# Kernel optimization log

Measured on AMD Instinct MI355X. Metric: run time of the kernel, lower is better.

The kernel has to match this reference:

```python
import jax, jax.numpy as jnp
import numpy as np

UNITS = 256


def setup_inputs() -> dict:
    key = jax.random.key(0)
    ks = jax.random.split(key, 9)
    B, H, W, C = 8, 64, 64, UNITS
    x = jax.random.normal(ks[0], (B, H, W, C), dtype=jnp.float32)
    # 1x1 Conv2D == per-pixel linear: weight [C_in, C_out], bias [C_out]
    def lin(k):
        return jax.random.normal(k, (C, UNITS), dtype=jnp.float32) * (2.0 / C) ** 0.5
    return {
        "x": x,
        "wq": lin(ks[1]), "bq": jnp.zeros((UNITS,), jnp.float32),
        "wk": lin(ks[2]), "bk": jnp.zeros((UNITS,), jnp.float32),
        "wv": lin(ks[3]), "bv": jnp.zeros((UNITS,), jnp.float32),
        "wp": lin(ks[4]), "bp": jnp.zeros((UNITS,), jnp.float32),
    }


def reference(x, wq, bq, wk, bk, wv, bv, wp, bp):
    B, H, W, C = x.shape
    N = H * W
    scale = jnp.asarray(UNITS, jnp.float32) ** -0.5
    xf = x.reshape(B, N, C)  # 1x1 conv == matmul over channels
    q = xf @ wq + bq
    k = xf @ wk + bk
    v = xf @ wv + bv
    # (b,h,w,c)x(b,H,W,c)->(b,h,w,H,W) flattened to (b,N,N)
    scores = jnp.einsum('bnc,bmc->bnm', q, k) * scale
    attn = jax.nn.softmax(scores, axis=-1)
    out = jnp.einsum('bnm,bmc->bnc', attn, v)
    proj = out @ wp + bp
    return x + proj.reshape(B, H, W, UNITS)
```

## Files before the change

kernel.cpp:

```cpp
#include <hip/hip_runtime.h>


typedef _Float16 half8 __attribute__((ext_vector_type(8)));
typedef _Float16 half4 __attribute__((ext_vector_type(4)));
typedef float f32x4 __attribute__((ext_vector_type(4)));
typedef float f32x16 __attribute__((ext_vector_type(16)));
typedef unsigned int u32x4 __attribute__((ext_vector_type(4)));
typedef unsigned int u32x2 __attribute__((ext_vector_type(2)));

#define MFMA16(a, b, c) __builtin_amdgcn_mfma_f32_16x16x32_f16((a), (b), (c), 0, 0, 0)
#define MFMA32(a, b, c) __builtin_amdgcn_mfma_f32_32x32x16_f16((a), (b), (c), 0, 0, 0)

#if __has_builtin(__builtin_amdgcn_exp2f)
#define EXP2(x) __builtin_amdgcn_exp2f(x)
#else
#define EXP2(x) exp2f(x)
#endif

#define QSCALE 0.09016843898f
#define ESHIFT 11.5415603f

__device__ __forceinline__ void lds_load16(const void* g, void* l) {
    __builtin_amdgcn_global_load_lds(
        (const __attribute__((address_space(1))) unsigned int*)g,
        (__attribute__((address_space(3))) unsigned int*)l, 16, 0, 0);
}

__global__ __launch_bounds__(256)
void wt_prep(const float* __restrict__ w0, const float* __restrict__ w1,
             const float* __restrict__ w2, const float* __restrict__ w3,
             _Float16* __restrict__ outw)
{
    __shared__ _Float16 sT[64 * 72];
    const int z = blockIdx.z;
    const float* W = (z == 0) ? w0 : (z == 1) ? w1 : (z == 2) ? w2 : w3;
    _Float16* O = outw + z * 65536;
    const int kb = blockIdx.x * 64, nb = blockIdx.y * 64;
    const int t = threadIdx.x;
    const int r = t >> 4, c4 = (t & 15) * 4;
#pragma unroll
    for (int i = 0; i < 4; ++i) {
        f32x4 ld = *(const f32x4*)(W + (size_t)(kb + r + i * 16) * 256 + nb + c4);
#pragma unroll
        for (int j = 0; j < 4; ++j) sT[(c4 + j) * 72 + r + i * 16] = (_Float16)ld[j];
    }
    __syncthreads();
#pragma unroll
    for (int i = 0; i < 4; ++i) {
        int n = r + i * 16;
        *(u32x2*)&O[(size_t)(nb + n) * 256 + kb + c4] = *(const u32x2*)&sT[n * 72 + c4];
    }
}

__global__ __launch_bounds__(256)
void qkv_gemm(const float* __restrict__ x, const _Float16* __restrict__ wt,
              const float* __restrict__ bq, const float* __restrict__ bk,
              const float* __restrict__ bv,
              _Float16* __restrict__ qo, _Float16* __restrict__ ko,
              _Float16* __restrict__ vo)
{
    __shared__ _Float16 smem[12800];

    const int tid  = threadIdx.x;
    const int w    = tid >> 6;
    const int lane = tid & 63;
    const int quad = lane >> 4;
    const int l16  = lane & 15;
    const int m0   = blockIdx.x * 128;
    const int n0   = blockIdx.y * 64;
    const int rA = tid >> 1, cA = (tid & 1) << 4;
    const int rB = tid >> 2, cB = (tid & 3) << 3;

    const float* ap = x + (size_t)(m0 + rA) * 256 + cA;
    f32x4 a0 = *(const f32x4*)ap,       a1 = *(const f32x4*)(ap + 4);
    f32x4 a2 = *(const f32x4*)(ap + 8), a3 = *(const f32x4*)(ap + 12);
    u32x4 bst[3];
#pragma unroll
    for (int o = 0; o < 3; ++o)
        bst[o] = *(const u32x4*)(wt + o * 65536 + (size_t)(n0 + rB) * 256 + cB);

    f32x4 zero4 = {0.f, 0.f, 0.f, 0.f};
    f32x4 acc[3][8];
#pragma unroll
    for (int o = 0; o < 3; ++o)
#pragma unroll
        for (int mt = 0; mt < 8; ++mt) acc[o][mt] = zero4;

    for (int it = 0; it < 8; ++it) {
        __syncthreads();
        half8 t0, t1;
#pragma unroll
        for (int j = 0; j < 4; ++j) {
            t0[j] = (_Float16)a0[j]; t0[j + 4] = (_Float16)a1[j];
            t1[j] = (_Float16)a2[j]; t1[j + 4] = (_Float16)a3[j];
        }
        *(half8*)&smem[rA * 40 + cA]     = t0;
        *(half8*)&smem[rA * 40 + cA + 8] = t1;
#pragma unroll
        for (int o = 0; o < 3; ++o)
            *(u32x4*)&smem[5120 + o * 2560 + rB * 40 + cB] = bst[o];
        __syncthreads();
        if (it < 7) {
            int k0 = (it + 1) * 32;
            const float* ap2 = x + (size_t)(m0 + rA) * 256 + k0 + cA;
            a0 = *(const f32x4*)ap2;       a1 = *(const f32x4*)(ap2 + 4);
            a2 = *(const f32x4*)(ap2 + 8); a3 = *(const f32x4*)(ap2 + 12);
#pragma unroll
            for (int o = 0; o < 3; ++o)
                bst[o] = *(const u32x4*)(wt + o * 65536 + (size_t)(n0 + rB) * 256 + k0 + cB);
        }
        half8 af[8];
#pragma unroll
        for (int mt = 0; mt < 8; ++mt)
            af[mt] = *(const half8*)&smem[(mt * 16 + l16) * 40 + quad * 8];
#pragma unroll
        for (int o = 0; o < 3; ++o) {
            half8 bf = *(const half8*)&smem[5120 + o * 2560 + (16 * w + l16) * 40 + quad * 8];
#pragma unroll
            for (int mt = 0; mt < 8; ++mt)
                acc[o][mt] = MFMA16(af[mt], bf, acc[o][mt]);
        }
    }

    const int col = n0 + 16 * w + l16;
#pragma unroll
    for (int mt = 0; mt < 8; ++mt) {
#pragma unroll
        for (int reg = 0; reg < 4; ++reg) {
            int row = m0 + 16 * mt + quad * 4 + reg;
            qo[(size_t)row * 256 + col] = (_Float16)((acc[0][mt][reg] + bq[col]) * QSCALE);
            ko[(size_t)row * 256 + col] = (_Float16)(acc[1][mt][reg] + bk[col]);
        }
    }
    __syncthreads();
    _Float16* sT = smem;
#pragma unroll
    for (int mt = 0; mt < 8; ++mt)
#pragma unroll
        for (int reg = 0; reg < 4; ++reg)
            sT[(16 * w + l16) * 136 + 16 * mt + quad * 4 + reg] =
                (_Float16)(acc[2][mt][reg] + bv[col]);
    __syncthreads();
    int ch = tid >> 2, po = (tid & 3) << 5;
    int bb = m0 >> 12, pix = m0 & 4095;
    _Float16* dst = vo + (size_t)bb * 1048576 + (size_t)(n0 + ch) * 4096 + pix + po;
#pragma unroll
    for (int i = 0; i < 4; ++i)
        *(u32x4*)(dst + i * 8) = *(const u32x4*)&sT[ch * 136 + po + i * 8];
}

__global__ __launch_bounds__(256)
void proj_gemm(const _Float16* __restrict__ opart, const float* __restrict__ lpart,
               const _Float16* __restrict__ Wt, const float* __restrict__ bias,
               const float* __restrict__ resid, float* __restrict__ out)
{
    __shared__ _Float16 smem[7680];
    _Float16* sB = smem + 5120;

    const int tid  = threadIdx.x;
    const int w    = tid >> 6;
    const int lane = tid & 63;
    const int quad = lane >> 4;
    const int l16  = lane & 15;
    const int m0   = blockIdx.x * 128;
    const int n0   = blockIdx.y * 64;
    const int rA = tid >> 1, cA = (tid & 1) << 4;
    const int rB = tid >> 2, cB = (tid & 3) << 3;

    const _Float16* o1p = opart;
    const _Float16* o2p = opart + 8388608;
    const int row = m0 + rA;
    const float inv = 1.0f / (lpart[row] + lpart[32768 + row]);

    u32x4 a1v = *(const u32x4*)(o1p + (size_t)row * 256 + cA);
    u32x4 a1w = *(const u32x4*)(o1p + (size_t)row * 256 + cA + 8);
    u32x4 a2v = *(const u32x4*)(o2p + (size_t)row * 256 + cA);
    u32x4 a2w = *(const u32x4*)(o2p + (size_t)row * 256 + cA + 8);
    u32x4 bst = *(const u32x4*)(Wt + (size_t)(n0 + rB) * 256 + cB);

    f32x4 zero4 = {0.f, 0.f, 0.f, 0.f};
    f32x4 acc[2][4];
#pragma unroll
    for (int m = 0; m < 2; ++m)
#pragma unroll
        for (int nt = 0; nt < 4; ++nt) acc[m][nt] = zero4;

    for (int it = 0; it < 8; ++it) {
        __syncthreads();
        {
            half8 h1 = *(half8*)&a1v, h2 = *(half8*)&a2v, t;
#pragma unroll
            for (int j = 0; j < 8; ++j)
                t[j] = (_Float16)(((float)h1[j] + (float)h2[j]) * inv);
            *(half8*)&smem[rA * 40 + cA] = t;
            half8 g1 = *(half8*)&a1w, g2 = *(half8*)&a2w, u;
#pragma unroll
            for (int j = 0; j < 8; ++j)
                u[j] = (_Float16)(((float)g1[j] + (float)g2[j]) * inv);
            *(half8*)&smem[rA * 40 + cA + 8] = u;
        }
        *(u32x4*)&sB[rB * 40 + cB] = bst;
        __syncthreads();
        if (it < 7) {
            int k0 = (it + 1) * 32;
            a1v = *(const u32x4*)(o1p + (size_t)row * 256 + k0 + cA);
            a1w = *(const u32x4*)(o1p + (size_t)row * 256 + k0 + cA + 8);
            a2v = *(const u32x4*)(o2p + (size_t)row * 256 + k0 + cA);
            a2w = *(const u32x4*)(o2p + (size_t)row * 256 + k0 + cA + 8);
            bst = *(const u32x4*)(Wt + (size_t)(n0 + rB) * 256 + k0 + cB);
        }
        half8 af[2];
#pragma unroll
        for (int m = 0; m < 2; ++m)
            af[m] = *(const half8*)&smem[((2 * w + m) * 16 + l16) * 40 + quad * 8];
#pragma unroll
        for (int nt = 0; nt < 4; ++nt) {
            half8 bf = *(const half8*)&sB[(nt * 16 + l16) * 40 + quad * 8];
#pragma unroll
            for (int m = 0; m < 2; ++m)
                acc[m][nt] = MFMA16(af[m], bf, acc[m][nt]);
        }
    }
#pragma unroll
    for (int m = 0; m < 2; ++m)
#pragma unroll
        for (int nt = 0; nt < 4; ++nt) {
#pragma unroll
            for (int reg = 0; reg < 4; ++reg) {
                int orow = m0 + (2 * w + m) * 16 + quad * 4 + reg;
                int col = n0 + nt * 16 + l16;
                out[(size_t)orow * 256 + col] =
                    acc[m][nt][reg] + bias[col] + resid[(size_t)orow * 256 + col];
            }
        }
}

__global__ __launch_bounds__(512, 2)
void attn_kernel(const _Float16* __restrict__ q, const _Float16* __restrict__ k,
                 const _Float16* __restrict__ vt, _Float16* __restrict__ opart,
                 float* __restrict__ lpart)
{
    extern __shared__ char smem[];
    char* sKb = smem;
    char* sVb = smem + 32768;

    const int tid  = threadIdx.x;
    const int w    = tid >> 6;
    const int lane = tid & 63;
    const int l31  = lane & 31;
    const int hi   = lane >> 5;
    const int bid  = blockIdx.x;
    const int xcd  = bid & 7, idx = bid >> 3;
    const int g    = xcd + 8 * (idx & 1);
    const int qg   = idx >> 1;
    const int b    = g >> 1;
    const int kh   = g & 1;

    const _Float16* kb = k  + (size_t)b * 1048576 + (size_t)kh * 524288;
    const _Float16* vb = vt + (size_t)b * 1048576 + kh * 2048;
    const int rowbase = qg * 256 + w * 32;

    half8 qf[16];
    {
        const _Float16* q0 = q + (size_t)(b * 4096 + rowbase + l31) * 256 + hi * 8;
#pragma unroll
        for (int s = 0; s < 16; ++s) qf[s] = *(const half8*)(q0 + s * 16);
    }

    f32x16 o[8];
#pragma unroll
    for (int i = 0; i < 8; ++i)
#pragma unroll
        for (int j = 0; j < 16; ++j) o[i][j] = 0.f;
    float ls = 0.f;

    const int koffL = l31 * 256 + hi * 8;

#pragma unroll
    for (int j = 0; j < 2; ++j) {
        int s = w * 2 + j;
        lds_load16(kb + koffL + s * 16, sKb + s * 1024);
        int ct = s >> 1, ks = s & 1;
        lds_load16(vb + (size_t)(32 * ct + l31) * 4096 + 16 * ks + 8 * hi,
                   sVb + s * 1024);
    }

    for (int kt = 0; kt < 64; ++kt) {
        const int p = kt & 1;
        __syncthreads();

        if (kt < 63) {
            const _Float16* ktb = kb + (size_t)(kt + 1) * 8192;
            const _Float16* vtb = vb + (kt + 1) * 32;
            char* dK = sKb + (1 - p) * 16384;
            char* dV = sVb + (1 - p) * 16384;
#pragma unroll
            for (int j = 0; j < 2; ++j) {
                int s = w * 2 + j;
                lds_load16(ktb + koffL + s * 16, dK + s * 1024);
                int ct = s >> 1, ks = s & 1;
                lds_load16(vtb + (size_t)(32 * ct + l31) * 4096 + 16 * ks + 8 * hi,
                           dV + s * 1024);
            }
        }

        const char* K = sKb + p * 16384;
        const char* V = sVb + p * 16384;

        f32x16 saA, saB;
#pragma unroll
        for (int j = 0; j < 16; ++j) { saA[j] = 0.f; saB[j] = 0.f; }
        __builtin_amdgcn_s_setprio(1);
#pragma unroll
        for (int s = 0; s < 16; s += 2) {
            half8 a0 = *(const half8*)(K + s * 1024 + lane * 16);
            half8 a1 = *(const half8*)(K + (s + 1) * 1024 + lane * 16);
            saA = MFMA32(a0, qf[s], saA);
            saB = MFMA32(a1, qf[s + 1], saB);
        }
        __builtin_amdgcn_s_setprio(0);

        unsigned int c[8];
#pragma unroll
        for (int j = 0; j < 8; ++j) saA[j] += saB[j];
#pragma unroll
        for (int qq = 0; qq < 2; ++qq) {
            float p0 = EXP2(saA[qq * 4 + 0] - ESHIFT);
            float p1 = EXP2(saA[qq * 4 + 1] - ESHIFT);
            float p2 = EXP2(saA[qq * 4 + 2] - ESHIFT);
            float p3 = EXP2(saA[qq * 4 + 3] - ESHIFT);
            ls += (p0 + p1) + (p2 + p3);
            c[2 * qq]     = __builtin_bit_cast(unsigned int,
                                __builtin_amdgcn_cvt_pkrtz(p0, p1));
            c[2 * qq + 1] = __builtin_bit_cast(unsigned int,
                                __builtin_amdgcn_cvt_pkrtz(p2, p3));
        }
        u32x2 s0 = __builtin_amdgcn_permlane32_swap(c[0], c[2], false, false);
        u32x2 s1 = __builtin_amdgcn_permlane32_swap(c[1], c[3], false, false);
        u32x4 w0 = {s0[0], s1[0], s0[1], s1[1]};
        half8 pf0 = __builtin_bit_cast(half8, w0);

        __builtin_amdgcn_s_setprio(1);
#pragma unroll
        for (int ct = 0; ct < 8; ++ct) {
            half8 b0 = *(const half8*)(V + (ct * 2 + 0) * 1024 + lane * 16);
            o[ct] = MFMA32(pf0, b0, o[ct]);
        }
        __builtin_amdgcn_s_setprio(0);

#pragma unroll
        for (int j = 8; j < 16; ++j) saA[j] += saB[j];
#pragma unroll
        for (int qq = 2; qq < 4; ++qq) {
            float p0 = EXP2(saA[qq * 4 + 0] - ESHIFT);
            float p1 = EXP2(saA[qq * 4 + 1] - ESHIFT);
            float p2 = EXP2(saA[qq * 4 + 2] - ESHIFT);
            float p3 = EXP2(saA[qq * 4 + 3] - ESHIFT);
            ls += (p0 + p1) + (p2 + p3);
            c[2 * qq]     = __builtin_bit_cast(unsigned int,
                                __builtin_amdgcn_cvt_pkrtz(p0, p1));
            c[2 * qq + 1] = __builtin_bit_cast(unsigned int,
                                __builtin_amdgcn_cvt_pkrtz(p2, p3));
        }
        u32x2 s2 = __builtin_amdgcn_permlane32_swap(c[4], c[6], false, false);
        u32x2 s3 = __builtin_amdgcn_permlane32_swap(c[5], c[7], false, false);
        u32x4 w1 = {s2[0], s3[0], s2[1], s3[1]};
        half8 pf1 = __builtin_bit_cast(half8, w1);

        __builtin_amdgcn_s_setprio(1);
#pragma unroll
        for (int ct = 0; ct < 8; ++ct) {
            half8 b1 = *(const half8*)(V + (ct * 2 + 1) * 1024 + lane * 16);
            o[ct] = MFMA32(pf1, b1, o[ct]);
        }
        __builtin_amdgcn_s_setprio(0);
    }

    ls += __shfl_xor(ls, 32);
    _Float16* po = opart + (size_t)kh * 8388608 + (size_t)(b * 4096 + rowbase) * 256;
    float* pl = lpart + kh * 32768 + b * 4096 + rowbase;
    if (hi == 0) pl[l31] = ls;
#pragma unroll
    for (int ct = 0; ct < 8; ++ct) {
#pragma unroll
        for (int reg = 0; reg < 16; ++reg) {
            int row = (reg & 3) + 8 * (reg >> 2) + 4 * hi;
            po[(size_t)row * 256 + ct * 32 + l31] = (_Float16)o[ct][reg];
        }
    }
}

extern "C" void kernel_launch(void* const* d_in, const int* in_sizes, int n_in,
                              void* d_out, int out_size, void* d_ws, size_t ws_size,
                              hipStream_t stream) {
    const float* x  = (const float*)d_in[0];
    const float* wq = (const float*)d_in[1];
    const float* bq = (const float*)d_in[2];
    const float* wk = (const float*)d_in[3];
    const float* bk = (const float*)d_in[4];
    const float* wv = (const float*)d_in[5];
    const float* bv = (const float*)d_in[6];
    const float* wp = (const float*)d_in[7];
    const float* bp = (const float*)d_in[8];

    _Float16* qws  = (_Float16*)d_ws;
    _Float16* kws  = qws + 8388608;
    _Float16* vtws = kws + 8388608;
    _Float16* ows  = vtws + 8388608;
    _Float16* wt   = ows + 16777216;
    float*    lws  = (float*)(wt + 262144);

    dim3 blk(256);

    (void)hipFuncSetAttribute((const void*)attn_kernel,
                              hipFuncAttributeMaxDynamicSharedMemorySize, 65536);

    wt_prep<<<dim3(4, 4, 4), blk, 0, stream>>>(wq, wk, wv, wp, wt);
    qkv_gemm<<<dim3(256, 4), blk, 0, stream>>>(x, wt, bq, bk, bv, qws, kws, vtws);
    attn_kernel<<<dim3(256), dim3(512), 65536, stream>>>(qws, kws, vtws, ows, lws);
    proj_gemm<<<dim3(256, 4), blk, 0, stream>>>(ows, lws, wt + 196608, bp, x, (float*)d_out);
}
```

Before: 282.5 us.

## Triple-buffer K/V tiles in attention with partial vmcnt waits

The attention kernel moves from double to triple buffering of K and V tiles in LDS, prefetching two tiles ahead. The full __syncthreads is replaced by an explicit s_waitcnt vmcnt(4) plus a raw barrier, so the newest in-flight tile load can stay outstanding while the current tile is consumed. This is meant to hide global-to-LDS latency better. In exchange, dynamic LDS grows to 96KB per block, which can limit how many blocks fit per CU. Correctness also depends on the hand-counted vmcnt matching the four loads each thread issues per stage.

```diff
diff --git a/kernel.cpp b/kernel.cpp
--- a/kernel.cpp
+++ b/kernel.cpp
@@ -242,7 +242,7 @@
 {
     extern __shared__ char smem[];
     char* sKb = smem;
-    char* sVb = smem + 32768;
+    char* sVb = smem + 49152;
 
     const int tid  = threadIdx.x;
     const int w    = tid >> 6;
@@ -276,36 +276,35 @@
 
     const int koffL = l31 * 256 + hi * 8;
 
-#pragma unroll
-    for (int j = 0; j < 2; ++j) {
-        int s = w * 2 + j;
-        lds_load16(kb + koffL + s * 16, sKb + s * 1024);
-        int ct = s >> 1, ks = s & 1;
-        lds_load16(vb + (size_t)(32 * ct + l31) * 4096 + 16 * ks + 8 * hi,
-                   sVb + s * 1024);
-    }
-
+    auto stage = [&](int t, char* dK, char* dV) {
+        const _Float16* ktb = kb + (size_t)t * 8192;
+        const _Float16* vtb = vb + t * 32;
+#pragma unroll
+        for (int j = 0; j < 2; ++j) {
+            int s = w * 2 + j;
+            lds_load16(ktb + koffL + s * 16, dK + s * 1024);
+            int ct = s >> 1, ks = s & 1;
+            lds_load16(vtb + (size_t)(32 * ct + l31) * 4096 + 16 * ks + 8 * hi,
+                       dV + s * 1024);
+        }
+    };
+
+    stage(0, sKb, sVb);
+    stage(1, sKb + 16384, sVb + 16384);
+
+    int cur = 0;
     for (int kt = 0; kt < 64; ++kt) {
-        const int p = kt & 1;
-        __syncthreads();
-
-        if (kt < 63) {
-            const _Float16* ktb = kb + (size_t)(kt + 1) * 8192;
-            const _Float16* vtb = vb + (kt + 1) * 32;
-            char* dK = sKb + (1 - p) * 16384;
-            char* dV = sVb + (1 - p) * 16384;
-#pragma unroll
-            for (int j = 0; j < 2; ++j) {
-                int s = w * 2 + j;
-                lds_load16(ktb + koffL + s * 16, dK + s * 1024);
-                int ct = s >> 1, ks = s & 1;
-                lds_load16(vtb + (size_t)(32 * ct + l31) * 4096 + 16 * ks + 8 * hi,
-                           dV + s * 1024);
-            }
-        }
-
-        const char* K = sKb + p * 16384;
-        const char* V = sVb + p * 16384;
+        if (kt < 63) { __asm__ volatile("s_waitcnt vmcnt(4)" ::: "memory"); }
+        else         { __asm__ volatile("s_waitcnt vmcnt(0)" ::: "memory"); }
+        __builtin_amdgcn_s_barrier();
+
+        if (kt < 62) {
+            int nb = cur + 2; if (nb >= 3) nb -= 3;
+            stage(kt + 2, sKb + nb * 16384, sVb + nb * 16384);
+        }
+
+        const char* K = sKb + cur * 16384;
+        const char* V = sVb + cur * 16384;
 
         f32x16 saA, saB;
 #pragma unroll
@@ -374,6 +373,8 @@
             o[ct] = MFMA32(pf1, b1, o[ct]);
         }
         __builtin_amdgcn_s_setprio(0);
+
+        cur = (cur + 1 == 3) ? 0 : cur + 1;
     }
 
     ls += __shfl_xor(ls, 32);
@@ -413,10 +414,10 @@
     dim3 blk(256);
 
     (void)hipFuncSetAttribute((const void*)attn_kernel,
-                              hipFuncAttributeMaxDynamicSharedMemorySize, 65536);
+                              hipFuncAttributeMaxDynamicSharedMemorySize, 98304);
 
     wt_prep<<<dim3(4, 4, 4), blk, 0, stream>>>(wq, wk, wv, wp, wt);
     qkv_gemm<<<dim3(256, 4), blk, 0, stream>>>(x, wt, bq, bk, bv, qws, kws, vtws);
-    attn_kernel<<<dim3(256), dim3(512), 65536, stream>>>(qws, kws, vtws, ows, lws);
+    attn_kernel<<<dim3(256), dim3(512), 98304, stream>>>(qws, kws, vtws, ows, lws);
     proj_gemm<<<dim3(256, 4), blk, 0, stream>>>(ows, lws, wt + 196608, bp, x, (float*)d_out);
 }
```

Result: no change. 282.6 us (+0.0%).
